# Performance work log

Measured on AMD Instinct MI355X. Metric: run time of the kernel, lower is better.

## Reference

```python
import jax, jax.numpy as jnp
import numpy as np
from jax import lax

BCE_WEIGHT = 0.5
DICE_WEIGHT = 0.5
BOUNDARY_WEIGHT = 3.0
KERNEL_SIZE = 3
SMOOTH = 1e-6
EPS = 1e-7  # clamp for log stability (torch BCE clamps log at -100)


def setup_inputs() -> dict:
    key = jax.random.key(0)
    k1, k2 = jax.random.split(key)
    B, C, H, W = 32, 1, 512, 512
    pred = jax.random.uniform(k1, (B, C, H, W), dtype=jnp.float32)
    target = jax.random.randint(k2, (B, C, H, W), 0, 2, dtype=jnp.int32)
    return {"pred": pred, "target": target}


def _extract_boundary(t):
    # cv2 dilate/erode with all-ones 3x3 kernel == 3x3 max/min pooling.
    # cv2 morphology border behavior (-inf for dilate, +inf for erode)
    # matches reduce_window identity padding with 'SAME'.
    k = KERNEL_SIZE
    win = (1, 1, k, k)
    one = (1, 1, 1, 1)
    dilated = lax.reduce_window(t, -jnp.inf, lax.max, win, one, 'SAME')
    eroded = lax.reduce_window(t, jnp.inf, lax.min, win, one, 'SAME')
    return dilated - eroded  # in {0,1} for binary masks


def reference(pred, target):
    t = target.astype(jnp.float32)  # (B,1,H,W) binary

    # Boundary-aware weighted BCE
    boundary = _extract_boundary(t)
    weights = jnp.where(boundary > 0, BOUNDARY_WEIGHT, 1.0)
    p = jnp.clip(pred, EPS, 1.0 - EPS)
    bce_map = -(t * jnp.log(p) + (1.0 - t) * jnp.log1p(-p))
    bce = jnp.mean(bce_map * weights)

    # Dice loss over flattened tensors
    pf = pred.reshape(-1)
    tf = t.reshape(-1)
    intersection = jnp.sum(pf * tf)
    dice_coef = (2.0 * intersection + SMOOTH) / (jnp.sum(pf) + jnp.sum(tf) + SMOOTH)
    dice = 1.0 - dice_coef

    total = BCE_WEIGHT * bce + DICE_WEIGHT * dice
    return total, bce, dice
```

## Files before the change

kernel.cpp:

```cpp
#include <hip/hip_runtime.h>


#define BB 32
#define HH 512
#define WW 512
#define N_TOTAL (BB * HH * WW)
#define SEG 8
#define W8 (WW / SEG)
#define NSEG (BB * HH * W8)
#define NBLK 2048

__global__ __launch_bounds__(256) void loss_main_kernel(
        const float* __restrict__ pred,
        const int* __restrict__ target,
        float4* __restrict__ partials) {
    float wbce = 0.f, inter = 0.f, sp = 0.f;
    int st_i = 0;

    const int lane = threadIdx.x & 63;
    const int stride = gridDim.x * blockDim.x;
    for (int seg = blockIdx.x * blockDim.x + threadIdx.x; seg < NSEG;
         seg += stride) {
        const int w0 = (seg & (W8 - 1)) << 3;
        const int h  = (seg >> 6) & (HH - 1);
        const int b  = seg >> 15;

        const size_t rowbase = ((size_t)(b * HH + h)) * WW;

        const float4 p0 = *(const float4*)(pred + rowbase + w0);
        const float4 p1 = *(const float4*)(pred + rowbase + w0 + 4);

        const int* rowC = target + rowbase;
        const int* rowU = (h > 0)      ? rowC - WW : rowC;
        const int* rowD = (h < HH - 1) ? rowC + WW : rowC;

        const int4 uA = *(const int4*)(rowU + w0);
        const int4 uB = *(const int4*)(rowU + w0 + 4);
        const int4 cA = *(const int4*)(rowC + w0);
        const int4 cB = *(const int4*)(rowC + w0 + 4);
        const int4 dA = *(const int4*)(rowD + w0);
        const int4 dB = *(const int4*)(rowD + w0 + 4);

        const int o0 = uA.x | cA.x | dA.x,  n0 = uA.x & cA.x & dA.x;
        const int o1 = uA.y | cA.y | dA.y,  n1 = uA.y & cA.y & dA.y;
        const int o2 = uA.z | cA.z | dA.z,  n2 = uA.z & cA.z & dA.z;
        const int o3 = uA.w | cA.w | dA.w,  n3 = uA.w & cA.w & dA.w;
        const int o4 = uB.x | cB.x | dB.x,  n4 = uB.x & cB.x & dB.x;
        const int o5 = uB.y | cB.y | dB.y,  n5 = uB.y & cB.y & dB.y;
        const int o6 = uB.z | cB.z | dB.z,  n6 = uB.z & cB.z & dB.z;
        const int o7 = uB.w | cB.w | dB.w,  n7 = uB.w & cB.w & dB.w;

        int oL = __shfl_up(o7, 1);
        int nL = __shfl_up(n7, 1);
        int oR = __shfl_down(o0, 1);
        int nR = __shfl_down(n0, 1);
        if (lane == 0)  { oL = o0; nL = n0; }
        if (lane == 63) { oR = o7; nR = n7; }

        const int e0 = (oL | o0 | o1) != (nL & n0 & n1);
        const int e1 = (o0 | o1 | o2) != (n0 & n1 & n2);
        const int e2 = (o1 | o2 | o3) != (n1 & n2 & n3);
        const int e3 = (o2 | o3 | o4) != (n2 & n3 & n4);
        const int e4 = (o3 | o4 | o5) != (n3 & n4 & n5);
        const int e5 = (o4 | o5 | o6) != (n4 & n5 & n6);
        const int e6 = (o5 | o6 | o7) != (n5 & n6 & n7);
        const int e7 = (o6 | o7 | oR) != (n6 & n7 & nR);

#define ACC(T, P, E)                                                   \
        {                                                              \
            const float pc = fminf(fmaxf((P), 1e-7f), 1.0f - 1e-7f);   \
            const float x  = (T) ? pc : (1.0f - pc);                   \
            wbce += ((E) ? 3.0f : 1.0f) * (-__logf(x));                \
            sp += (P);                                                 \
            if (T) inter += (P);                                       \
            st_i += (T);                                               \
        }

        ACC(cA.x, p0.x, e0); ACC(cA.y, p0.y, e1);
        ACC(cA.z, p0.z, e2); ACC(cA.w, p0.w, e3);
        ACC(cB.x, p1.x, e4); ACC(cB.y, p1.y, e5);
        ACC(cB.z, p1.z, e6); ACC(cB.w, p1.w, e7);
#undef ACC
    }

    float st = (float)st_i;
    #pragma unroll
    for (int off = 32; off > 0; off >>= 1) {
        wbce  += __shfl_down(wbce,  off);
        inter += __shfl_down(inter, off);
        sp    += __shfl_down(sp,    off);
        st    += __shfl_down(st,    off);
    }

    __shared__ float smem[4][4];
    const int wave = threadIdx.x >> 6;
    if ((threadIdx.x & 63) == 0) {
        smem[wave][0] = wbce; smem[wave][1] = inter;
        smem[wave][2] = sp;   smem[wave][3] = st;
    }
    __syncthreads();
    if (threadIdx.x == 0) {
        float s0 = 0, s1 = 0, s2 = 0, s3 = 0;
        #pragma unroll
        for (int wv = 0; wv < 4; ++wv) {
            s0 += smem[wv][0]; s1 += smem[wv][1];
            s2 += smem[wv][2]; s3 += smem[wv][3];
        }
        partials[blockIdx.x] = make_float4(s0, s1, s2, s3);
    }
}

__global__ __launch_bounds__(1024) void finalize_kernel(
        const float4* __restrict__ partials, float* __restrict__ out) {
    double a0 = 0, a1 = 0, a2 = 0, a3 = 0;
    #pragma unroll
    for (int k = 0; k < NBLK / 1024; ++k) {
        const float4 p = partials[k * 1024 + threadIdx.x];
        a0 += p.x; a1 += p.y; a2 += p.z; a3 += p.w;
    }
    #pragma unroll
    for (int off = 32; off > 0; off >>= 1) {
        a0 += __shfl_down(a0, off);
        a1 += __shfl_down(a1, off);
        a2 += __shfl_down(a2, off);
        a3 += __shfl_down(a3, off);
    }
    __shared__ double smem[16][4];
    const int wave = threadIdx.x >> 6;
    if ((threadIdx.x & 63) == 0) {
        smem[wave][0] = a0; smem[wave][1] = a1;
        smem[wave][2] = a2; smem[wave][3] = a3;
    }
    __syncthreads();
    if (threadIdx.x == 0) {
        double s0 = 0, s1 = 0, s2 = 0, s3 = 0;
        #pragma unroll
        for (int wv = 0; wv < 16; ++wv) {
            s0 += smem[wv][0]; s1 += smem[wv][1];
            s2 += smem[wv][2]; s3 += smem[wv][3];
        }
        const double bce = s0 / (double)N_TOTAL;
        const double dice_coef = (2.0 * s1 + 1e-6) / (s2 + s3 + 1e-6);
        const double dice = 1.0 - dice_coef;
        const double total = 0.5 * bce + 0.5 * dice;
        out[0] = (float)total;
        out[1] = (float)bce;
        out[2] = (float)dice;
    }
}

extern "C" void kernel_launch(void* const* d_in, const int* in_sizes, int n_in,
                              void* d_out, int out_size, void* d_ws, size_t ws_size,
                              hipStream_t stream) {
    const float* pred  = (const float*)d_in[0];
    const int* target  = (const int*)d_in[1];
    float* out = (float*)d_out;
    float4* partials = (float4*)d_ws;

    loss_main_kernel<<<NBLK, 256, 0, stream>>>(pred, target, partials);
    finalize_kernel<<<1, 1024, 0, stream>>>(partials, out);
}
```

Measured before the change: 23.07 us.

## Replace grid-stride loop with fixed two-iteration unrolled loop and XCD-aware block swizzle

Each thread now handles exactly two segments, 16 batches apart, in a fully unrolled loop instead of a grid-stride loop. Row offsets are computed once and kept in 32-bit arithmetic. Block IDs are remapped so consecutive hardware block indices, which are spread round-robin across XCDs, cover contiguous row ranges, aiming for better L2 reuse of the neighbouring target rows. The unrolling also lets the loads of both iterations be issued together for more memory-level parallelism. In exchange, the kernel is hardcoded to the grid size and shape.

```diff
diff --git a/kernel.cpp b/kernel.cpp
--- a/kernel.cpp
+++ b/kernel.cpp
@@ -5,41 +5,46 @@
 #define HH 512
 #define WW 512
 #define N_TOTAL (BB * HH * WW)
-#define SEG 8
-#define W8 (WW / SEG)
-#define NSEG (BB * HH * W8)
 #define NBLK 2048
 
 __global__ __launch_bounds__(256) void loss_main_kernel(
         const float* __restrict__ pred,
         const int* __restrict__ target,
         float4* __restrict__ partials) {
+    const int lane = threadIdx.x & 63;
+
+    const int bid = ((int)blockIdx.x & 7) * (NBLK / 8) + ((int)blockIdx.x >> 3);
+
+    const int seg = bid * 256 + (int)threadIdx.x;
+    const int w0  = (seg & 63) << 3;
+    const int h   = (seg >> 6) & (HH - 1);
+    const int b   = seg >> 15;
+
+    const int offC = (b * HH + h) * WW + w0;
+    const int dU = (h > 0)      ? -WW : 0;
+    const int dD = (h < HH - 1) ?  WW : 0;
+
     float wbce = 0.f, inter = 0.f, sp = 0.f;
     int st_i = 0;
 
-    const int lane = threadIdx.x & 63;
-    const int stride = gridDim.x * blockDim.x;
-    for (int seg = blockIdx.x * blockDim.x + threadIdx.x; seg < NSEG;
-         seg += stride) {
-        const int w0 = (seg & (W8 - 1)) << 3;
-        const int h  = (seg >> 6) & (HH - 1);
-        const int b  = seg >> 15;
+    #pragma unroll
+    for (int it = 0; it < 2; ++it) {
+        const int base = offC + it * (16 * HH * WW);
 
-        const size_t rowbase = ((size_t)(b * HH + h)) * WW;
+        const float* pp = pred + base;
+        const int*   tC = target + base;
+        const int*   tU = target + base + dU;
+        const int*   tD = target + base + dD;
 
-        const float4 p0 = *(const float4*)(pred + rowbase + w0);
-        const float4 p1 = *(const float4*)(pred + rowbase + w0 + 4);
+        const float4 p0 = *(const float4*)(pp);
+        const float4 p1 = *(const float4*)(pp + 4);
 
-        const int* rowC = target + rowbase;
-        const int* rowU = (h > 0)      ? rowC - WW : rowC;
-        const int* rowD = (h < HH - 1) ? rowC + WW : rowC;
-
-        const int4 uA = *(const int4*)(rowU + w0);
-        const int4 uB = *(const int4*)(rowU + w0 + 4);
-        const int4 cA = *(const int4*)(rowC + w0);
-        const int4 cB = *(const int4*)(rowC + w0 + 4);
-        const int4 dA = *(const int4*)(rowD + w0);
-        const int4 dB = *(const int4*)(rowD + w0 + 4);
+        const int4 uA = *(const int4*)(tU);
+        const int4 uB = *(const int4*)(tU + 4);
+        const int4 cA = *(const int4*)(tC);
+        const int4 cB = *(const int4*)(tC + 4);
+        const int4 dA = *(const int4*)(tD);
+        const int4 dB = *(const int4*)(tD + 4);
 
         const int o0 = uA.x | cA.x | dA.x,  n0 = uA.x & cA.x & dA.x;
         const int o1 = uA.y | cA.y | dA.y,  n1 = uA.y & cA.y & dA.y;
```

New measurement: 21.25 us. -7.9%, faster.
